# Optimization experiments

Measured on AMD Instinct MI355X. Metric: run time of the kernel, lower is better.

The kernel has to match this reference:

```python
import jax, jax.numpy as jnp
import numpy as np
import math

N_HEAD = 16
HEAD_DIM = 64
LN_EPS = 1e-5
TEMP = 1.0

def _layernorm(x, scale, bias):
    # normalize over last dim (head_dim)
    mu = jnp.mean(x, axis=-1, keepdims=True)
    var = jnp.mean(jnp.square(x - mu), axis=-1, keepdims=True)
    return (x - mu) / jnp.sqrt(var + LN_EPS) * scale + bias

def setup_inputs() -> dict:
    key = jax.random.key(0)
    ks = jax.random.split(key, 3)
    B, S, C = 4, 2048, 1024
    x = jax.random.normal(ks[0], (B, S, C), dtype=jnp.float32)
    w_qkv = jax.random.normal(ks[1], (C, 3 * C), dtype=jnp.float32) * (C ** -0.5)
    w_proj = jax.random.normal(ks[2], (C, C), dtype=jnp.float32) * (C ** -0.5)
    return {
        "x": x,
        "w_qkv": w_qkv,
        "w_proj": w_proj,
        "q_scale": jnp.ones((HEAD_DIM,), jnp.float32),
        "q_bias": jnp.zeros((HEAD_DIM,), jnp.float32),
        "k_scale": jnp.ones((HEAD_DIM,), jnp.float32),
        "k_bias": jnp.zeros((HEAD_DIM,), jnp.float32),
    }

def reference(x, w_qkv, w_proj, q_scale, q_bias, k_scale, k_bias):
    B, S, C = x.shape
    H, D = N_HEAD, HEAD_DIM
    # qkv projection -> [B,S,3,H,D] -> [3,B,H,S,D]
    qkv = (x @ w_qkv).reshape(B, S, 3, H, D).transpose(2, 0, 3, 1, 4)
    q = _layernorm(qkv[0], q_scale, q_bias)
    k = _layernorm(qkv[1], k_scale, k_bias)
    v = qkv[2]
    # temperature-scaled logits, stable softmax
    inv = 1.0 / (math.sqrt(D) * max(TEMP, 1e-6))
    logits = jnp.einsum('bhqd,bhkd->bhqk', q, k) * inv
    att = jax.nn.softmax(logits, axis=-1)
    # entropy stats (track_stats=True path)
    s_raw = -jnp.sum(att * jnp.log(att + 1e-9), axis=-1)  # [B,H,S]
    batch_entropies = jnp.mean(s_raw / math.log(S), axis=(1, 2))  # [B]
    out = jnp.einsum('bhqk,bhkd->bhqd', att, v).transpose(0, 2, 1, 3).reshape(B, S, C)
    return out @ w_proj, batch_entropies
```

## Files before the change

### kernel.cpp

```cpp
#include <hip/hip_runtime.h>
#include <hip/hip_bf16.h>
#include <math.h>

#define CB 4
#define CS 2048
#define CC 1024
#define CH 16
#define CD 64
#define CBS (CB*CS)

typedef unsigned short u16;
typedef __bf16 bf16x8 __attribute__((ext_vector_type(8)));
typedef float f32x4 __attribute__((ext_vector_type(4)));
typedef float f32x16 __attribute__((ext_vector_type(16)));
typedef unsigned short u16x4 __attribute__((ext_vector_type(4)));
typedef unsigned short u16x8 __attribute__((ext_vector_type(8)));
typedef unsigned u32x2 __attribute__((ext_vector_type(2)));

__device__ __forceinline__ u16 f2bf(float f){
  union { float f; unsigned u; } v; v.f = f;
  unsigned r = v.u + 0x7FFFu + ((v.u >> 16) & 1u);
  return (u16)(r >> 16);
}
__device__ __forceinline__ unsigned pack2bf(float a, float b){
  __hip_bfloat162 h = __float22bfloat162_rn(make_float2(a, b));
  union { __hip_bfloat162 h; unsigned u; } c; c.h = h; return c.u;
}
__device__ __forceinline__ f32x4 mfma16(bf16x8 a, bf16x8 b, f32x4 c){
  return __builtin_amdgcn_mfma_f32_16x16x32_bf16(a, b, c, 0, 0, 0);
}
__device__ __forceinline__ f32x16 mfma32(bf16x8 a, bf16x8 b, f32x16 c){
  return __builtin_amdgcn_mfma_f32_32x32x16_bf16(a, b, c, 0, 0, 0);
}
__device__ __forceinline__ void gload16(const u16* g, u16* lds_base_uniform){
  __builtin_amdgcn_global_load_lds(
      (const __attribute__((address_space(1))) unsigned int*)g,
      (__attribute__((address_space(3))) unsigned int*)lds_base_uniform, 16, 0, 0);
}

__global__ __launch_bounds__(256) void convert_x_kernel(
    const float* __restrict__ x, u16* __restrict__ xb, float* __restrict__ zero4){
  if (blockIdx.x == 0 && threadIdx.x < 4) zero4[threadIdx.x] = 0.0f;
  size_t i = ((size_t)blockIdx.x*256 + threadIdx.x)*8;
  float4 a = *(const float4*)(x+i);
  float4 b = *(const float4*)(x+i+4);
  u16x8 o = { f2bf(a.x),f2bf(a.y),f2bf(a.z),f2bf(a.w),
              f2bf(b.x),f2bf(b.y),f2bf(b.z),f2bf(b.w) };
  *(u16x8*)(xb+i) = o;
}

template<int K, int N>
__global__ __launch_bounds__(256) void transpose_convert_kernel(
    const float* __restrict__ w, u16* __restrict__ wt){
  __shared__ u16 tile[64][65];
  const int nb = N/64;
  int tk0 = (blockIdx.x / nb) * 64;
  int tn0 = (blockIdx.x % nb) * 64;
  int t = threadIdx.x;
  for (int i = 0; i < 4; i++) {
    int r = i*16 + (t>>4);
    int c = (t&15)*4;
    float4 v = *(const float4*)(w + (size_t)(tk0+r)*N + tn0 + c);
    tile[c+0][r]=f2bf(v.x); tile[c+1][r]=f2bf(v.y);
    tile[c+2][r]=f2bf(v.z); tile[c+3][r]=f2bf(v.w);
  }
  __syncthreads();
  for (int i = 0; i < 4; i++) {
    int r = i*16 + (t>>4);
    int c = (t&15)*4;
    u16x4 o = { tile[r][c+0], tile[r][c+1], tile[r][c+2], tile[r][c+3] };
    *(u16x4*)(wt + (size_t)(tn0+r)*K + tk0 + c) = o;
  }
}

__global__ __launch_bounds__(256, 3) void gemm_qkv_ln_kernel(
    const u16* __restrict__ xb, const u16* __restrict__ wqkvT,
    const float* __restrict__ qsc, const float* __restrict__ qbi,
    const float* __restrict__ ksc, const float* __restrict__ kbi,
    u16* __restrict__ qb, u16* __restrict__ kb, u16* __restrict__ vtb){
  __shared__ __align__(16) u16 bl[3][128*32];
  int t = threadIdx.x;
  int wv = t >> 6, lane = t & 63, lo = lane & 15, q4 = lane >> 4;
  int m0 = blockIdx.x * 128;
  int n0 = blockIdx.y * 128;
  int lsB = (lane & 3) ^ ((lane >> 3) & 3);
  const u16* bg0  = wqkvT + (size_t)(n0 + (lane>>2))*CC + lsB*8;
  const u16* agl0 = xb + (size_t)(m0 + wv*32 + lo)*CC + q4*8;
  const u16* agl1 = agl0 + (size_t)16*CC;

  f32x4 acc[2][8];
  #pragma unroll
  for (int i=0;i<2;i++)
    #pragma unroll
    for (int j=0;j<8;j++) acc[i][j] = (f32x4){0.f,0.f,0.f,0.f};

  auto stageB = [&](int buf, int kk){
    #pragma unroll
    for (int cc=0; cc<2; cc++){
      int c = wv*2 + cc;
      gload16(bg0 + (size_t)c*16*CC + kk*32, &bl[buf][c*512]);
    }
  };

  stageB(0, 0);
  stageB(1, 1);
  bf16x8 acur0 = *(const bf16x8*)(agl0);
  bf16x8 acur1 = *(const bf16x8*)(agl1);
  int cur = 0;
  const int akey = (lo >> 1) & 3;

  for (int kk = 0; kk < 32; kk++){
    if (kk < 30){
      asm volatile("s_waitcnt vmcnt(4)" ::: "memory");
      __builtin_amdgcn_s_barrier();
      __builtin_amdgcn_sched_barrier(0);
      int nb = cur + 2; if (nb >= 3) nb -= 3;
      stageB(nb, kk + 2);
    } else if (kk == 30){
      asm volatile("s_waitcnt vmcnt(4)" ::: "memory");
      __builtin_amdgcn_s_barrier();
      __builtin_amdgcn_sched_barrier(0);
    } else {
      asm volatile("s_waitcnt vmcnt(0)" ::: "memory");
      __builtin_amdgcn_s_barrier();
      __builtin_amdgcn_sched_barrier(0);
    }
    bf16x8 anxt0, anxt1;
    if (kk < 31){
      anxt0 = *(const bf16x8*)(agl0 + (kk+1)*32);
      anxt1 = *(const bf16x8*)(agl1 + (kk+1)*32);
    } else {
      anxt0 = acur0; anxt1 = acur1;
    }
    const u16* bc = &bl[cur][0];
    int soff = (q4 ^ akey) << 3;
    __builtin_amdgcn_s_setprio(1);
    #pragma unroll
    for (int nt=0; nt<8; nt++){
      bf16x8 b = *(const bf16x8*)&bc[(nt*16 + lo)*32 + soff];
      acc[0][nt] = mfma16(acur0, b, acc[0][nt]);
      acc[1][nt] = mfma16(acur1, b, acc[1][nt]);
    }
    __builtin_amdgcn_s_setprio(0);
    acur0 = anxt0; acur1 = anxt1;
    cur = (cur == 2) ? 0 : cur + 1;
  }

  int three = n0 >> 10;
  int h0 = (n0 & 1023) >> 6;
  int bb = m0 >> 11, ss0 = m0 & (CS-1);

  if (three < 2){
    const float* scp = (three == 0) ? qsc : ksc;
    const float* bip = (three == 0) ? qbi : kbi;
    float outscale = (three == 0) ? 0.125f * 1.44269504088896f : 1.0f;
    u16* dst = (three == 0) ? qb : kb;

    for (int rt = 0; rt < 2; rt++){
      int tg = m0 + wv*32 + rt*16 + q4*4;
      for (int hf = 0; hf < 2; hf++){
        int h = h0 + hf;
        for (int r = 0; r < 4; r++){
          int token = tg + r;
          int ss = token & (CS-1);
          size_t base = (((size_t)(bb*CH + h))*CS + ss)*CD;
          float s1 = 0.f, s2 = 0.f;
          for (int j=0;j<4;j++){ float v = acc[rt][hf*4+j][r]; s1 += v; s2 += v*v; }
          for (int off=8; off>=1; off>>=1){
            s1 += __shfl_xor(s1, off, 16);
            s2 += __shfl_xor(s2, off, 16);
          }
          float mean = s1 * (1.f/64.f);
          float var  = s2 * (1.f/64.f) - mean*mean;
          float rstd = rsqrtf(var + 1e-5f);
          for (int j=0;j<4;j++){
            int d = j*16 + lo;
            float v = (acc[rt][hf*4+j][r] - mean) * rstd * scp[d] + bip[d];
            dst[base + d] = f2bf(v * outscale);
          }
        }
      }
    }
  } else {
    u16* tl = (u16*)&bl[0][0];
    for (int hf = 0; hf < 2; hf++){
      __syncthreads();
      #pragma unroll
      for (int rt = 0; rt < 2; rt++){
        int tok = wv*32 + rt*16 + q4*4;
        #pragma unroll
        for (int j = 0; j < 4; j++){
          int d = j*16 + lo;
          #pragma unroll
          for (int r = 0; r < 4; r++)
            tl[d*132 + tok + r] = f2bf(acc[rt][hf*4+j][r]);
        }
      }
      __syncthreads();
      int h = h0 + hf;
      u16* vt = vtb + (((size_t)(bb*CH + h))*CD)*CS + ss0;
      int row = t >> 2, c0 = (t & 3) * 32;
      #pragma unroll
      for (int cc = 0; cc < 32; cc += 8){
        u16x8 o;
        #pragma unroll
        for (int jj=0;jj<8;jj++) o[jj] = tl[row*132 + c0 + cc + jj];
        *(u16x8*)(vt + (size_t)row*CS + c0 + cc) = o;
      }
    }
  }
}

__global__ __launch_bounds__(256, 2) void attention_kernel(
    const u16* __restrict__ qb, const u16* __restrict__ kb,
    const u16* __restrict__ vtb, u16* __restrict__ attnb, float* __restrict__ ent){
  __shared__ __align__(16) u16 kl[3][32*64];
  __shared__ __align__(16) u16 vl[3][64*32];
  int t = threadIdx.x;
  int wv = t >> 6, lane = t & 63;
  int col = lane & 31, hi = lane >> 5;
  int n = blockIdx.x;
  int xc = n & 7, j = n >> 3;
  int bh = xc + 8*(j >> 4);
  int qt = j & 15;
  int bI = bh >> 4;
  int q0w = qt*128 + wv*32;
  const u16* qbp = qb  + (size_t)bh * CS * CD;
  const u16* kbp = kb  + (size_t)bh * CS * CD;
  const u16* vbp = vtb + (size_t)bh * CD * CS;

  int srow8  = lane >> 3, sl8 = lane & 7;
  int srow16 = lane >> 2, sl4 = lane & 3;

  bf16x8 qf[4];
  #pragma unroll
  for (int ks=0;ks<4;ks++)
    qf[ks] = *(const bf16x8*)(qbp + (size_t)(q0w + col)*CD + ks*16 + hi*8);

  f32x16 o[2];
  #pragma unroll
  for (int nt=0;nt<2;nt++)
    #pragma unroll
    for (int i=0;i<16;i++) o[nt][i] = 0.f;
  float zacc = 0.f, tacc = 0.f;

  auto stage = [&](int buf, int tile){
    int skn = tile*32;
    int krow  = wv*8 + srow8;
    int kslot = sl8 ^ srow8 ^ wv;
    gload16(kbp + (size_t)(skn + krow)*CD + kslot*8, &kl[buf][wv*512]);
    int vrow  = wv*16 + srow16;
    int vslot = sl4 ^ (srow16 & 3);
    gload16(vbp + (size_t)vrow*CS + skn + vslot*8, &vl[buf][wv*512]);
  };

  stage(0, 0);
  stage(1, 1);

  const int kkey = (col & 7) ^ (col >> 3);
  const int vkey = (col & 3);
  int cur = 0;

  for (int it = 0; it < 64; it++){
    if (it < 62){
      asm volatile("s_waitcnt vmcnt(2)" ::: "memory");
      __builtin_amdgcn_s_barrier();
      __builtin_amdgcn_sched_barrier(0);
      int nb = cur + 2; if (nb >= 3) nb -= 3;
      stage(nb, it + 2);
    } else if (it == 62){
      asm volatile("s_waitcnt vmcnt(2)" ::: "memory");
      __builtin_amdgcn_s_barrier();
      __builtin_amdgcn_sched_barrier(0);
    } else {
      asm volatile("s_waitcnt vmcnt(0)" ::: "memory");
      __builtin_amdgcn_s_barrier();
      __builtin_amdgcn_sched_barrier(0);
    }
    const u16* kc = &kl[cur][0];
    const u16* vc = &vl[cur][0];

    bf16x8 kfr[4], vfr[2][2];
    #pragma unroll
    for (int ks=0;ks<4;ks++)
      kfr[ks] = *(const bf16x8*)&kc[col*64 + (((2*ks+hi) ^ kkey)<<3)];
    #pragma unroll
    for (int nt=0;nt<2;nt++)
      #pragma unroll
      for (int ks=0;ks<2;ks++)
        vfr[nt][ks] = *(const bf16x8*)&vc[(nt*32+col)*32 + (((ks*2+hi) ^ vkey)<<3)];

    f32x16 sf;
    #pragma unroll
    for (int i=0;i<16;i++) sf[i] = 0.f;
    __builtin_amdgcn_s_setprio(1);
    #pragma unroll
    for (int ks=0;ks<4;ks++)
      sf = mfma32(kfr[ks], qf[ks], sf);
    __builtin_amdgcn_s_setprio(0);

    #pragma unroll
    for (int ksl=0; ksl<2; ksl++){
      float p[2][4];
      #pragma unroll
      for (int gg=0; gg<2; gg++){
        int g = 2*ksl + gg;
        float l0 = sf[g*4+0], l1 = sf[g*4+1],
              l2 = sf[g*4+2], l3 = sf[g*4+3];
        float p0 = __builtin_amdgcn_exp2f(l0);
        float p1 = __builtin_amdgcn_exp2f(l1);
        float p2 = __builtin_amdgcn_exp2f(l2);
        float p3 = __builtin_amdgcn_exp2f(l3);
        zacc += (p0+p1)+(p2+p3);
        tacc += (p0*l0+p1*l1)+(p2*l2+p3*l3);
        p[gg][0]=p0; p[gg][1]=p1; p[gg][2]=p2; p[gg][3]=p3;
      }
      unsigned x0 = pack2bf(p[0][0], p[0][1]);
      unsigned x1 = pack2bf(p[0][2], p[0][3]);
      unsigned y0 = pack2bf(p[1][0], p[1][1]);
      unsigned y1 = pack2bf(p[1][2], p[1][3]);
      u32x2 s0 = __builtin_amdgcn_permlane32_swap(x0, y0, false, false);
      u32x2 s1 = __builtin_amdgcn_permlane32_swap(x1, y1, false, false);
      union { unsigned u[4]; bf16x8 v; } ap;
      ap.u[0] = s0[0]; ap.u[1] = s1[0]; ap.u[2] = s0[1]; ap.u[3] = s1[1];
      __builtin_amdgcn_s_setprio(1);
      o[0] = mfma32(ap.v, vfr[0][ksl], o[0]);
      o[1] = mfma32(ap.v, vfr[1][ksl], o[1]);
      __builtin_amdgcn_s_setprio(0);
    }
    cur = (cur == 2) ? 0 : cur + 1;
  }

  float z2 = zacc + __shfl_xor(zacc, 32);
  float t2 = tacc + __shfl_xor(tacc, 32);
  float invz = 1.f / z2;

  float srowv = 0.69314718055995f * (__builtin_amdgcn_logf(z2) - t2 * invz);
  float ev = (hi == 0) ? srowv : 0.f;
  for (int off=1; off<=32; off<<=1) ev += __shfl_xor(ev, off);
  if (lane == 0){
    float entscale = 1.0f / ((float)CH * (float)CS * logf((float)CS));
    atomicAdd(&ent[bI], ev * entscale);
  }

  float izv[4][4];
  #pragma unroll
  for (int g=0; g<4; g++)
    #pragma unroll
    for (int r=0; r<4; r++)
      izv[g][r] = __shfl(invz, 8*g + 4*hi + r);

  u16* obase = attnb + ((size_t)bh*CS + q0w)*CD;
  #pragma unroll
  for (int nt=0;nt<2;nt++){
    #pragma unroll
    for (int g=0;g<4;g++){
      #pragma unroll
      for (int r=0;r<4;r++){
        int qrow = 8*g + 4*hi + r;
        obase[(size_t)qrow*CD + nt*32 + col] = f2bf(o[nt][g*4+r] * izv[g][r]);
      }
    }
  }
}

__global__ __launch_bounds__(256, 3) void gemm_out_kernel(
    const u16* __restrict__ attnH, const u16* __restrict__ wprojT,
    float* __restrict__ out){
  __shared__ __align__(16) u16 bl[3][128*32];
  int t = threadIdx.x;
  int wv = t >> 6, lane = t & 63, lo = lane & 15, q4 = lane >> 4;
  int m0 = blockIdx.x * 128;
  int n0 = blockIdx.y * 128;
  int b  = m0 >> 11, s0 = m0 & (CS-1);
  int lsB = (lane & 3) ^ ((lane >> 3) & 3);
  const u16* bg0 = wprojT + (size_t)(n0 + (lane>>2))*CC + lsB*8;
  const u16* agl0 = attnH + ((size_t)(b*CH)*CS + s0 + wv*32 + lo)*CD + q4*8;
  const u16* agl1 = agl0 + (size_t)16*CD;

  f32x4 acc[2][8];
  #pragma unroll
  for (int i=0;i<2;i++)
    #pragma unroll
    for (int j=0;j<8;j++) acc[i][j] = (f32x4){0.f,0.f,0.f,0.f};

  auto aoff = [&](int kk) -> size_t {
    return (size_t)(kk >> 1)*CS*CD + (size_t)(kk & 1)*32;
  };
  auto stageB = [&](int buf, int kk){
    #pragma unroll
    for (int cc=0; cc<2; cc++){
      int c = wv*2 + cc;
      gload16(bg0 + (size_t)c*16*CC + kk*32, &bl[buf][c*512]);
    }
  };

  stageB(0, 0);
  stageB(1, 1);
  bf16x8 acur0 = *(const bf16x8*)(agl0);
  bf16x8 acur1 = *(const bf16x8*)(agl1);
  int cur = 0;
  const int akey = (lo >> 1) & 3;

  for (int kk = 0; kk < 32; kk++){
    if (kk < 30){
      asm volatile("s_waitcnt vmcnt(4)" ::: "memory");
      __builtin_amdgcn_s_barrier();
      __builtin_amdgcn_sched_barrier(0);
      int nb = cur + 2; if (nb >= 3) nb -= 3;
      stageB(nb, kk + 2);
    } else if (kk == 30){
      asm volatile("s_waitcnt vmcnt(4)" ::: "memory");
      __builtin_amdgcn_s_barrier();
      __builtin_amdgcn_sched_barrier(0);
    } else {
      asm volatile("s_waitcnt vmcnt(0)" ::: "memory");
      __builtin_amdgcn_s_barrier();
      __builtin_amdgcn_sched_barrier(0);
    }
    bf16x8 anxt0, anxt1;
    if (kk < 31){
      size_t ao = aoff(kk + 1);
      anxt0 = *(const bf16x8*)(agl0 + ao);
      anxt1 = *(const bf16x8*)(agl1 + ao);
    } else {
      anxt0 = acur0; anxt1 = acur1;
    }
    const u16* bc = &bl[cur][0];
    int soff = (q4 ^ akey) << 3;
    __builtin_amdgcn_s_setprio(1);
    #pragma unroll
    for (int nt=0; nt<8; nt++){
      bf16x8 b2 = *(const bf16x8*)&bc[(nt*16 + lo)*32 + soff];
      acc[0][nt] = mfma16(acur0, b2, acc[0][nt]);
      acc[1][nt] = mfma16(acur1, b2, acc[1][nt]);
    }
    __builtin_amdgcn_s_setprio(0);
    acur0 = anxt0; acur1 = anxt1;
    cur = (cur == 2) ? 0 : cur + 1;
  }

  for (int rt=0;rt<2;rt++){
    for (int r=0;r<4;r++){
      int row = m0 + wv*32 + rt*16 + q4*4 + r;
      for (int nt=0;nt<8;nt++)
        out[(size_t)row*CC + n0 + nt*16 + lo] = acc[rt][nt][r];
    }
  }
}

extern "C" void kernel_launch(void* const* d_in, const int* in_sizes, int n_in,
                              void* d_out, int out_size, void* d_ws, size_t ws_size,
                              hipStream_t stream) {
  const float* x      = (const float*)d_in[0];
  const float* w_qkv  = (const float*)d_in[1];
  const float* w_proj = (const float*)d_in[2];
  const float* q_scale= (const float*)d_in[3];
  const float* q_bias = (const float*)d_in[4];
  const float* k_scale= (const float*)d_in[5];
  const float* k_bias = (const float*)d_in[6];
  float* out = (float*)d_out;
  float* ent = out + (size_t)CBS * CC;

  u16* xb     = (u16*)d_ws;
  u16* wqkvT  = xb     + (size_t)CBS*CC;
  u16* wprojT = wqkvT  + (size_t)3*CC*CC;
  u16* qb     = wprojT + (size_t)CC*CC;
  u16* kb     = qb  + (size_t)CB*CH*CS*CD;
  u16* vbT    = kb  + (size_t)CB*CH*CS*CD;
  u16* attn   = xb;

  convert_x_kernel<<<dim3(CBS*CC/(256*8)), 256, 0, stream>>>(x, xb, ent);
  transpose_convert_kernel<CC, 3*CC><<<dim3((CC/64)*(3*CC/64)), 256, 0, stream>>>(w_qkv, wqkvT);
  transpose_convert_kernel<CC, CC><<<dim3((CC/64)*(CC/64)), 256, 0, stream>>>(w_proj, wprojT);
  gemm_qkv_ln_kernel<<<dim3(CBS/128, 3*CC/128), 256, 0, stream>>>(
      xb, wqkvT, q_scale, q_bias, k_scale, k_bias, qb, kb, vbT);
  attention_kernel<<<dim3(CB*CH*(CS/128)), 256, 0, stream>>>(qb, kb, vbT, attn, ent);
  gemm_out_kernel<<<dim3(CBS/128, CC/128), 256, 0, stream>>>(attn, wprojT, out);
}
```

Baseline: 323.3 us.

## Use 2x2 warp tiling in QKV and output GEMMs

Both GEMM kernels change from each wave covering 32 rows by 128 columns to a 2x2 wave grid where each wave covers 64 rows by 64 columns. This halves the LDS B-fragment reads per wave and balances the A/B register footprint, keeping the MFMA count per wave unchanged. The cost is twice as many global A loads per wave, so the vmcnt thresholds are raised to match. In the V-transpose epilogue only the matching half of the waves write to LDS on each pass.

```diff
diff --git a/kernel.cpp b/kernel.cpp
--- a/kernel.cpp
+++ b/kernel.cpp
@@ -81,18 +81,21 @@
   __shared__ __align__(16) u16 bl[3][128*32];
   int t = threadIdx.x;
   int wv = t >> 6, lane = t & 63, lo = lane & 15, q4 = lane >> 4;
+  int wm = wv >> 1, wn = wv & 1;
   int m0 = blockIdx.x * 128;
   int n0 = blockIdx.y * 128;
   int lsB = (lane & 3) ^ ((lane >> 3) & 3);
-  const u16* bg0  = wqkvT + (size_t)(n0 + (lane>>2))*CC + lsB*8;
-  const u16* agl0 = xb + (size_t)(m0 + wv*32 + lo)*CC + q4*8;
-  const u16* agl1 = agl0 + (size_t)16*CC;
-
-  f32x4 acc[2][8];
-  #pragma unroll
-  for (int i=0;i<2;i++)
-    #pragma unroll
-    for (int j=0;j<8;j++) acc[i][j] = (f32x4){0.f,0.f,0.f,0.f};
+  const u16* bg0 = wqkvT + (size_t)(n0 + (lane>>2))*CC + lsB*8;
+  const u16* agl[4];
+  #pragma unroll
+  for (int rt=0; rt<4; rt++)
+    agl[rt] = xb + (size_t)(m0 + wm*64 + rt*16 + lo)*CC + q4*8;
+
+  f32x4 acc[4][4];
+  #pragma unroll
+  for (int i=0;i<4;i++)
+    #pragma unroll
+    for (int j=0;j<4;j++) acc[i][j] = (f32x4){0.f,0.f,0.f,0.f};
 
   auto stageB = [&](int buf, int kk){
     #pragma unroll
@@ -104,80 +107,84 @@
 
   stageB(0, 0);
   stageB(1, 1);
-  bf16x8 acur0 = *(const bf16x8*)(agl0);
-  bf16x8 acur1 = *(const bf16x8*)(agl1);
+  bf16x8 acur[4];
+  #pragma unroll
+  for (int rt=0; rt<4; rt++) acur[rt] = *(const bf16x8*)(agl[rt]);
   int cur = 0;
   const int akey = (lo >> 1) & 3;
 
   for (int kk = 0; kk < 32; kk++){
     if (kk < 30){
-      asm volatile("s_waitcnt vmcnt(4)" ::: "memory");
+      asm volatile("s_waitcnt vmcnt(6)" ::: "memory");
       __builtin_amdgcn_s_barrier();
       __builtin_amdgcn_sched_barrier(0);
       int nb = cur + 2; if (nb >= 3) nb -= 3;
       stageB(nb, kk + 2);
     } else if (kk == 30){
+      asm volatile("s_waitcnt vmcnt(6)" ::: "memory");
+      __builtin_amdgcn_s_barrier();
+      __builtin_amdgcn_sched_barrier(0);
+    } else {
       asm volatile("s_waitcnt vmcnt(4)" ::: "memory");
       __builtin_amdgcn_s_barrier();
       __builtin_amdgcn_sched_barrier(0);
+    }
+    bf16x8 anxt[4];
+    if (kk < 31){
+      #pragma unroll
+      for (int rt=0; rt<4; rt++) anxt[rt] = *(const bf16x8*)(agl[rt] + (kk+1)*32);
     } else {
-      asm volatile("s_waitcnt vmcnt(0)" ::: "memory");
-      __builtin_amdgcn_s_barrier();
-      __builtin_amdgcn_sched_barrier(0);
-    }
-    bf16x8 anxt0, anxt1;
-    if (kk < 31){
-      anxt0 = *(const bf16x8*)(agl0 + (kk+1)*32);
-      anxt1 = *(const bf16x8*)(agl1 + (kk+1)*32);
-    } else {
-      anxt0 = acur0; anxt1 = acur1;
+      #pragma unroll
+      for (int rt=0; rt<4; rt++) anxt[rt] = acur[rt];
     }
     const u16* bc = &bl[cur][0];
     int soff = (q4 ^ akey) << 3;
     __builtin_amdgcn_s_setprio(1);
     #pragma unroll
-    for (int nt=0; nt<8; nt++){
-      bf16x8 b = *(const bf16x8*)&bc[(nt*16 + lo)*32 + soff];
-      acc[0][nt] = mfma16(acur0, b, acc[0][nt]);
-      acc[1][nt] = mfma16(acur1, b, acc[1][nt]);
+    for (int nt=0; nt<4; nt++){
+      bf16x8 b = *(const bf16x8*)&bc[(wn*64 + nt*16 + lo)*32 + soff];
+      acc[0][nt] = mfma16(acur[0], b, acc[0][nt]);
+      acc[1][nt] = mfma16(acur[1], b, acc[1][nt]);
+      acc[2][nt] = mfma16(acur[2], b, acc[2][nt]);
+      acc[3][nt] = mfma16(acur[3], b, acc[3][nt]);
     }
     __builtin_amdgcn_s_setprio(0);
-    acur0 = anxt0; acur1 = anxt1;
+    #pragma unroll
+    for (int rt=0; rt<4; rt++) acur[rt] = anxt[rt];
     cur = (cur == 2) ? 0 : cur + 1;
   }
 
   int three = n0 >> 10;
   int h0 = (n0 & 1023) >> 6;
-  int bb = m0 >> 11, ss0 = m0 & (CS-1);
+  int bb = m0 >> 11;
+  int ss0 = m0 & (CS-1);
 
   if (three < 2){
     const float* scp = (three == 0) ? qsc : ksc;
     const float* bip = (three == 0) ? qbi : kbi;
     float outscale = (three == 0) ? 0.125f * 1.44269504088896f : 1.0f;
     u16* dst = (three == 0) ? qb : kb;
-
-    for (int rt = 0; rt < 2; rt++){
-      int tg = m0 + wv*32 + rt*16 + q4*4;
-      for (int hf = 0; hf < 2; hf++){
-        int h = h0 + hf;
-        for (int r = 0; r < 4; r++){
-          int token = tg + r;
-          int ss = token & (CS-1);
-          size_t base = (((size_t)(bb*CH + h))*CS + ss)*CD;
-          float s1 = 0.f, s2 = 0.f;
-          for (int j=0;j<4;j++){ float v = acc[rt][hf*4+j][r]; s1 += v; s2 += v*v; }
-          for (int off=8; off>=1; off>>=1){
-            s1 += __shfl_xor(s1, off, 16);
-            s2 += __shfl_xor(s2, off, 16);
-          }
-          float mean = s1 * (1.f/64.f);
-          float var  = s2 * (1.f/64.f) - mean*mean;
-          float rstd = rsqrtf(var + 1e-5f);
-          for (int j=0;j<4;j++){
-            int d = j*16 + lo;
-            float v = (acc[rt][hf*4+j][r] - mean) * rstd * scp[d] + bip[d];
-            dst[base + d] = f2bf(v * outscale);
-          }
+    int h = h0 + wn;
+
+    for (int rt = 0; rt < 4; rt++){
+      int tg = m0 + wm*64 + rt*16 + q4*4;
+      for (int r = 0; r < 4; r++){
+        int token = tg + r;
+        int ss = token & (CS-1);
+        size_t base = (((size_t)(bb*CH + h))*CS + ss)*CD;
+        float s1 = 0.f, s2 = 0.f;
+        for (int nt=0;nt<4;nt++){ float v = acc[rt][nt][r]; s1 += v; s2 += v*v; }
+        for (int off=8; off>=1; off>>=1){
+          s1 += __shfl_xor(s1, off, 16);
+          s2 += __shfl_xor(s2, off, 16);
+        }
+        float mean = s1 * (1.f/64.f);
+        float var  = s2 * (1.f/64.f) - mean*mean;
+        float rstd = rsqrtf(var + 1e-5f);
+        for (int nt=0;nt<4;nt++){
+          int d = nt*16 + lo;
+          float v = (acc[rt][nt][r] - mean) * rstd * scp[d] + bip[d];
+          dst[base + d] = f2bf(v * outscale);
         }
       }
     }
@@ -185,15 +192,17 @@
     u16* tl = (u16*)&bl[0][0];
     for (int hf = 0; hf < 2; hf++){
       __syncthreads();
-      #pragma unroll
-      for (int rt = 0; rt < 2; rt++){
-        int tok = wv*32 + rt*16 + q4*4;
+      if (wn == hf){
         #pragma unroll
-        for (int j = 0; j < 4; j++){
-          int d = j*16 + lo;
+        for (int rt = 0; rt < 4; rt++){
+          int tok = wm*64 + rt*16 + q4*4;
           #pragma unroll
-          for (int r = 0; r < 4; r++)
-            tl[d*132 + tok + r] = f2bf(acc[rt][hf*4+j][r]);
+          for (int nt = 0; nt < 4; nt++){
+            int d = nt*16 + lo;
+            #pragma unroll
+            for (int r = 0; r < 4; r++)
+              tl[d*132 + tok + r] = f2bf(acc[rt][nt][r]);
+          }
         }
       }
       __syncthreads();
@@ -370,19 +379,22 @@
   __shared__ __align__(16) u16 bl[3][128*32];
   int t = threadIdx.x;
   int wv = t >> 6, lane = t & 63, lo = lane & 15, q4 = lane >> 4;
+  int wm = wv >> 1, wn = wv & 1;
   int m0 = blockIdx.x * 128;
   int n0 = blockIdx.y * 128;
   int b  = m0 >> 11, s0 = m0 & (CS-1);
   int lsB = (lane & 3) ^ ((lane >> 3) & 3);
   const u16* bg0 = wprojT + (size_t)(n0 + (lane>>2))*CC + lsB*8;
-  const u16* agl0 = attnH + ((size_t)(b*CH)*CS + s0 + wv*32 + lo)*CD + q4*8;
-  const u16* agl1 = agl0 + (size_t)16*CD;
-
-  f32x4 acc[2][8];
-  #pragma unroll
-  for (int i=0;i<2;i++)
-    #pragma unroll
-    for (int j=0;j<8;j++) acc[i][j] = (f32x4){0.f,0.f,0.f,0.f};
+  const u16* agl[4];
+  #pragma unroll
+  for (int rt=0; rt<4; rt++)
+    agl[rt] = attnH + ((size_t)(b*CH)*CS + s0 + wm*64 + rt*16 + lo)*CD + q4*8;
+
+  f32x4 acc[4][4];
+  #pragma unroll
+  for (int i=0;i<4;i++)
+    #pragma unroll
+    for (int j=0;j<4;j++) acc[i][j] = (f32x4){0.f,0.f,0.f,0.f};
 
   auto aoff = [&](int kk) -> size_t {
     return (size_t)(kk >> 1)*CS*CD + (size_t)(kk & 1)*32;
@@ -397,54 +409,59 @@
 
   stageB(0, 0);
   stageB(1, 1);
-  bf16x8 acur0 = *(const bf16x8*)(agl0);
-  bf16x8 acur1 = *(const bf16x8*)(agl1);
+  bf16x8 acur[4];
+  #pragma unroll
+  for (int rt=0; rt<4; rt++) acur[rt] = *(const bf16x8*)(agl[rt]);
   int cur = 0;
   const int akey = (lo >> 1) & 3;
 
   for (int kk = 0; kk < 32; kk++){
     if (kk < 30){
-      asm volatile("s_waitcnt vmcnt(4)" ::: "memory");
+      asm volatile("s_waitcnt vmcnt(6)" ::: "memory");
       __builtin_amdgcn_s_barrier();
       __builtin_amdgcn_sched_barrier(0);
       int nb = cur + 2; if (nb >= 3) nb -= 3;
       stageB(nb, kk + 2);
     } else if (kk == 30){
+      asm volatile("s_waitcnt vmcnt(6)" ::: "memory");
+      __builtin_amdgcn_s_barrier();
+      __builtin_amdgcn_sched_barrier(0);
+    } else {
       asm volatile("s_waitcnt vmcnt(4)" ::: "memory");
       __builtin_amdgcn_s_barrier();
       __builtin_amdgcn_sched_barrier(0);
-    } else {
-      asm volatile("s_waitcnt vmcnt(0)" ::: "memory");
-      __builtin_amdgcn_s_barrier();
-      __builtin_amdgcn_sched_barrier(0);
-    }
-    bf16x8 anxt0, anxt1;
+    }
+    bf16x8 anxt[4];
     if (kk < 31){
       size_t ao = aoff(kk + 1);
-      anxt0 = *(const bf16x8*)(agl0 + ao);
-      anxt1 = *(const bf16x8*)(agl1 + ao);
+      #pragma unroll
+      for (int rt=0; rt<4; rt++) anxt[rt] = *(const bf16x8*)(agl[rt] + ao);
     } else {
-      anxt0 = acur0; anxt1 = acur1;
+      #pragma unroll
+      for (int rt=0; rt<4; rt++) anxt[rt] = acur[rt];
     }
     const u16* bc = &bl[cur][0];
     int soff = (q4 ^ akey) << 3;
     __builtin_amdgcn_s_setprio(1);
     #pragma unroll
-    for (int nt=0; nt<8; nt++){
-      bf16x8 b2 = *(const bf16x8*)&bc[(nt*16 + lo)*32 + soff];
-      acc[0][nt] = mfma16(acur0, b2, acc[0][nt]);
-      acc[1][nt] = mfma16(acur1, b2, acc[1][nt]);
+    for (int nt=0; nt<4; nt++){
+      bf16x8 b2 = *(const bf16x8*)&bc[(wn*64 + nt*16 + lo)*32 + soff];
+      acc[0][nt] = mfma16(acur[0], b2, acc[0][nt]);
+      acc[1][nt] = mfma16(acur[1], b2, acc[1][nt]);
+      acc[2][nt] = mfma16(acur[2], b2, acc[2][nt]);
+      acc[3][nt] = mfma16(acur[3], b2, acc[3][nt]);
     }
     __builtin_amdgcn_s_setprio(0);
-    acur0 = anxt0; acur1 = anxt1;
+    #pragma unroll
+    for (int rt=0; rt<4; rt++) acur[rt] = anxt[rt];
     cur = (cur == 2) ? 0 : cur + 1;
   }
 
-  for (int rt=0;rt<2;rt++){
+  for (int rt=0;rt<4;rt++){
     for (int r=0;r<4;r++){
-      int row = m0 + wv*32 + rt*16 + q4*4 + r;
-      for (int nt=0;nt<8;nt++)
-        out[(size_t)row*CC + n0 + nt*16 + lo] = acc[rt][nt][r];
+      int row = m0 + wm*64 + rt*16 + q4*4 + r;
+      for (int nt=0;nt<4;nt++)
+        out[(size_t)row*CC + n0 + wn*64 + nt*16 + lo] = acc[rt][nt][r];
     }
   }
 }
```

Measured after the change: 370.7 us. +14.7%, slower.
